# Kernel tuning notes

Hardware: AMD Instinct MI355X
Metric: run time of the kernel (lower is better)

## Reference

```python
import jax, jax.numpy as jnp
import numpy as np

N_NODES, N_EDGES, B = 5000, 160000, 8
IN_DIM, NB, RH = 64, 8, 64
MUL0, MUL1, MUL2 = 32, 16, 8
NW = 144  # 32*3 + 16*2 + 8*2 tensor-product path weights per edge
R_MAX, AVG_NEI = 6.0, 32.0
NL, POOL_H, OUT_D = 4, 128, 512


def setup_inputs():
    ks = jax.random.split(jax.random.key(0), 24)
    f = lambda k, shape, scale=1.0: jax.random.normal(k, shape, jnp.float32) * scale
    return {
        "x": f(ks[0], (N_NODES, IN_DIM)),
        "pos": f(ks[1], (N_NODES, 3)),
        "W_in": f(ks[2], (IN_DIM, MUL0), IN_DIM ** -0.5),
        "Wr1": f(ks[3], (NL, NB, RH), NB ** -0.5), "br1": jnp.zeros((NL, RH)),
        "Wr2": f(ks[4], (NL, RH, RH), RH ** -0.5), "br2": jnp.zeros((NL, RH)),
        "Wr3": f(ks[5], (NL, RH, NW), RH ** -0.5), "br3": jnp.zeros((NL, NW)),
        "Wm0": f(ks[6], (NL, 56, MUL0), 56 ** -0.5),
        "Wm1": f(ks[7], (NL, 48, MUL1), 48 ** -0.5),
        "Wm2": f(ks[8], (NL, 40, MUL2), 40 ** -0.5),
        "Ws0": f(ks[9], (NL, MUL0, MUL0), MUL0 ** -0.5),
        "Ws1": f(ks[10], (NL, MUL1, MUL1), MUL1 ** -0.5),
        "Ws2": f(ks[11], (NL, MUL2, MUL2), MUL2 ** -0.5),
        "Wg": f(ks[12], (NL, MUL0, MUL1 + MUL2), MUL0 ** -0.5), "bg": jnp.zeros((NL, MUL1 + MUL2)),
        "Wp1": f(ks[13], (MUL0, POOL_H), MUL0 ** -0.5), "bp1": jnp.zeros((POOL_H,)),
        "Wp2": f(ks[14], (POOL_H, POOL_H), POOL_H ** -0.5), "bp2": jnp.zeros((POOL_H,)),
        "Wp3": f(ks[15], (POOL_H, 1), POOL_H ** -0.5), "bp3": jnp.zeros((1,)),
        "Wo1": f(ks[16], (MUL0, OUT_D * 2), MUL0 ** -0.5), "bo1": jnp.zeros((OUT_D * 2,)),
        "g1": jnp.ones((OUT_D * 2,)), "be1": jnp.zeros((OUT_D * 2,)),
        "Wo2": f(ks[17], (OUT_D * 2, OUT_D), (OUT_D * 2) ** -0.5), "bo2": jnp.zeros((OUT_D,)),
        "g2": jnp.ones((OUT_D,)), "be2": jnp.zeros((OUT_D,)),
        "edge_index": jax.random.randint(ks[18], (2, N_EDGES), 0, N_NODES),
        "batch": jnp.sort(jax.random.randint(ks[19], (N_NODES,), 0, B)),
    }


def _ln(x, gamma, beta):
    m = x.mean(-1, keepdims=True)
    v = x.var(-1, keepdims=True)
    return (x - m) / jnp.sqrt(v + 1e-5) * gamma + beta


def _forward(x, pos, W_in, Wr1, br1, Wr2, br2, Wr3, br3, Wm0, Wm1, Wm2,
             Ws0, Ws1, Ws2, Wg, bg, Wp1, bp1, Wp2, bp2, Wp3, bp3,
             Wo1, bo1, g1, be1, Wo2, bo2, g2, be2, edge_index, batch):
    N = x.shape[0]
    src, dst = edge_index[0], edge_index[1]
    vec = pos[src] - pos[dst]                       # [E,3]
    r = jnp.sqrt(jnp.sum(vec * vec, -1) + 1e-12)    # [E]
    u = vec / r[:, None]
    # Bessel radial basis with smooth polynomial cutoff (p=6)
    nfreq = jnp.arange(1, NB + 1, dtype=x.dtype)
    bess = jnp.sqrt(2.0 / R_MAX) * jnp.sin(nfreq * jnp.pi * r[:, None] / R_MAX) / r[:, None]
    t = jnp.clip(r / R_MAX, 0.0, 1.0)
    fcut = (1.0 - 28.0 * t**6 + 48.0 * t**7 - 21.0 * t**8) * (r < R_MAX).astype(x.dtype)
    edge_emb = bess * fcut[:, None]                 # [E,NB]
    # real spherical harmonics of edge direction, component normalization
    ux, uy, uz = u[:, 0], u[:, 1], u[:, 2]
    Y1 = jnp.sqrt(3.0) * u                          # [E,3]
    Y2 = jnp.stack([15.0**0.5 * ux * uy, 15.0**0.5 * uy * uz,
                    0.5 * 5.0**0.5 * (3.0 * uz * uz - 1.0),
                    15.0**0.5 * ux * uz, 0.5 * 15.0**0.5 * (ux * ux - uy * uy)], -1)  # [E,5]
    # input embedding: 64x0e -> hidden irreps (only scalar path exists; l>0 start at 0)
    s = x @ W_in                                    # [N,32]
    v = jnp.zeros((N, MUL1, 3), x.dtype)            # [N,16,3] 1o
    q = jnp.zeros((N, MUL2, 5), x.dtype)            # [N,8,5]  2e
    for i in range(NL):
        w = jax.nn.silu(edge_emb @ Wr1[i] + br1[i])
        w = jax.nn.silu(w @ Wr2[i] + br2[i])
        w = w @ Wr3[i] + br3[i]                     # [E,144] per-edge TP path weights
        w_ss, w_sv, w_sq, w_vs, w_vv, w_qs, w_qq = jnp.split(w, [32, 64, 96, 112, 128, 136], -1)
        se, ve, qe = s[src], v[src], q[src]         # gather
        # tensor-product messages, grouped by output irrep
        m0 = jnp.concatenate([w_ss * se,
                              w_vv * jnp.einsum('ecm,em->ec', ve, Y1) / 3.0**0.5,
                              w_qq * jnp.einsum('ecm,em->ec', qe, Y2) / 5.0**0.5], -1)   # [E,56]
        m1 = jnp.concatenate([(w_sv * se)[:, :, None] * Y1[:, None, :],
                              w_vs[:, :, None] * ve], 1)                                  # [E,48,3]
        m2 = jnp.concatenate([(w_sq * se)[:, :, None] * Y2[:, None, :],
                              w_qs[:, :, None] * qe], 1)                                  # [E,40,5]
        a0 = jax.ops.segment_sum(m0, dst, num_segments=N) / AVG_NEI
        a1 = jax.ops.segment_sum(m1, dst, num_segments=N) / AVG_NEI
        a2 = jax.ops.segment_sum(m2, dst, num_segments=N) / AVG_NEI
        # per-irrep linear mix + self-connection
        ns = a0 @ Wm0[i] + s @ Ws0[i]
        nv = jnp.einsum('ncm,co->nom', a1, Wm1[i]) + jnp.einsum('ncm,co->nom', v, Ws1[i])
        nq = jnp.einsum('ncm,co->nom', a2, Wm2[i]) + jnp.einsum('ncm,co->nom', q, Ws2[i])
        # gate activation + resnet
        gates = jax.nn.sigmoid(ns @ Wg[i] + bg[i])  # [N,24]
        s = s + jax.nn.silu(ns)
        v = v + nv * gates[:, :MUL1, None]
        q = q + nq * gates[:, MUL1:, None]
    # attention pooling over scalar channels (scatter-softmax per graph)
    logits = (jax.nn.silu(jax.nn.silu(s @ Wp1 + bp1) @ Wp2 + bp2) @ Wp3 + bp3)[:, 0]
    mx = jax.ops.segment_max(logits, batch, num_segments=B)
    z = jnp.exp(logits - mx[batch])
    att = z / jax.ops.segment_sum(z, batch, num_segments=B)[batch]
    gpool = jax.ops.segment_sum(s * att[:, None], batch, num_segments=B)  # [B,32]
    h = jax.nn.silu(_ln(gpool @ Wo1 + bo1, g1, be1))
    return _ln(h @ Wo2 + bo2, g2, be2)              # [B,512]


def reference(x, pos, W_in, Wr1, br1, Wr2, br2, Wr3, br3, Wm0, Wm1, Wm2,
              Ws0, Ws1, Ws2, Wg, bg, Wp1, bp1, Wp2, bp2, Wp3, bp3,
              Wo1, bo1, g1, be1, Wo2, bo2, g2, be2, edge_index, batch):
    return _forward(x, pos, W_in, Wr1, br1, Wr2, br2, Wr3, br3, Wm0, Wm1, Wm2,
                    Ws0, Ws1, Ws2, Wg, bg, Wp1, bp1, Wp2, bp2, Wp3, bp3,
                    Wo1, bo1, g1, be1, Wo2, bo2, g2, be2, edge_index, batch)
```

## Files before the change

kernel.cpp:

```cpp
#include <hip/hip_runtime.h>

constexpr int NN  = 5000;
constexpr int NE  = 160000;
constexpr int NB_ = 8;
constexpr float RMAX   = 6.0f;
constexpr float INV_AVG = 1.0f/32.0f;
constexpr float SQ3  = 1.7320508075688772f;
constexpr float ISQ3 = 0.5773502691896258f;
constexpr float ISQ5 = 0.4472135954999579f;
constexpr float SQ15 = 3.872983346207417f;
constexpr float SQ5  = 2.2360679774997896f;
constexpr float PIF  = 3.14159265358979323846f;

__device__ __forceinline__ float sigmoid_f(float x){
#if __has_builtin(__builtin_amdgcn_rcpf)
    return __builtin_amdgcn_rcpf(1.0f + __expf(-x));
#else
    return 1.0f / (1.0f + __expf(-x));
#endif
}
__device__ __forceinline__ float silu_f(float x){ return x * sigmoid_f(x); }

__global__ void k_geom(const float* __restrict__ pos, const int* __restrict__ ei,
                       float* __restrict__ geom, int* __restrict__ counts){
    int e = blockIdx.x*256 + threadIdx.x;
    if (e >= NE) return;
    int s = ei[e], d = ei[NE + e];
    float vx = pos[3*s]-pos[3*d], vy = pos[3*s+1]-pos[3*d+1], vz = pos[3*s+2]-pos[3*d+2];
    float r2 = vx*vx + vy*vy + vz*vz + 1e-12f;
    float r  = sqrtf(r2);
    float ir = 1.0f/r;
    float ux = vx*ir, uy = vy*ir, uz = vz*ir;
    float t  = fminf(r*(1.0f/RMAX), 1.0f);
    float t2=t*t, t3=t2*t, t6=t3*t3, t7=t6*t, t8=t7*t;
    float fc = (1.0f - 28.0f*t6 + 48.0f*t7 - 21.0f*t8) * (r < RMAX ? 1.0f : 0.0f);
    float cb = sqrtf(2.0f/RMAX) * ir * fc;
    float w[16];
    #pragma unroll
    for (int k=0;k<8;k++){
        float arg = (float)(k+1) * (PIF/RMAX) * r;
        w[k] = cb * sinf(arg);
    }
    w[8]  = SQ3*ux; w[9] = SQ3*uy; w[10] = SQ3*uz;
    w[11] = SQ15*ux*uy; w[12] = SQ15*uy*uz; w[13] = 0.5f*SQ5*(3.0f*uz*uz-1.0f);
    w[14] = SQ15*ux*uz; w[15] = 0.5f*SQ15*(ux*ux-uy*uy);
    float4* o = (float4*)(geom + (size_t)e*16);
    o[0] = make_float4(w[0],w[1],w[2],w[3]);
    o[1] = make_float4(w[4],w[5],w[6],w[7]);
    o[2] = make_float4(w[8],w[9],w[10],w[11]);
    o[3] = make_float4(w[12],w[13],w[14],w[15]);
    atomicAdd(&counts[d], 1);
}

__global__ void k_scan(int* __restrict__ cr, int* __restrict__ fpos){
    __shared__ int part[256];
    int t = threadIdx.x;
    const int CH = (NN + 255)/256;
    int base = t*CH;
    int s = 0;
    for (int i=0;i<CH;i++){ int idx = base+i; if (idx < NN) s += cr[idx]; }
    part[t] = s; __syncthreads();
    for (int off=1; off<256; off<<=1){
        int v = (t >= off) ? part[t-off] : 0;
        __syncthreads();
        part[t] += v;
        __syncthreads();
    }
    int run = (t==0) ? 0 : part[t-1];
    for (int i=0;i<CH;i++){
        int idx = base+i;
        if (idx < NN){
            int c = cr[idx];
            cr[idx]  = run;
            fpos[idx] = run;
            run += c;
        } else if (idx == NN){
            cr[idx] = run;
        }
    }
}

__global__ void k_fill(const int* __restrict__ ei, int* __restrict__ fpos,
                       int* __restrict__ elist, int* __restrict__ slot){
    int e = blockIdx.x*256 + threadIdx.x;
    if (e >= NE) return;
    int d = ei[NE+e];
    int p = atomicAdd(&fpos[d], 1);
    elist[p] = e;
    slot[e]  = p;
}

__global__ void k_sinit(const float* __restrict__ x, const float* __restrict__ Win,
                        float* __restrict__ sA){
    int tid = blockIdx.x*256 + threadIdx.x;
    int n = tid >> 5, o = tid & 31;
    if (n >= NN) return;
    float a = 0.f;
    #pragma unroll
    for (int k=0;k<64;k++) a = fmaf(x[n*64+k], Win[k*32+o], a);
    sA[n*32+o] = a;
}

__launch_bounds__(256)
__global__ void k_mlp(const float* __restrict__ geom, const int* __restrict__ slot,
                      const float* __restrict__ Wr1, const float* __restrict__ br1,
                      const float* __restrict__ Wr2, const float* __restrict__ br2,
                      const float* __restrict__ Wr3, const float* __restrict__ br3,
                      float* __restrict__ wbuf, int layer){
    int e = blockIdx.x*256 + threadIdx.x;
    if (e >= NE) return;
    const float* W1 = Wr1 + layer*(8*64);
    const float* b1 = br1 + layer*64;
    const float* W2 = Wr2 + layer*(64*64);
    const float* b2 = br2 + layer*64;
    const float* W3 = Wr3 + layer*(64*144);
    const float* b3 = br3 + layer*144;
    float4 ga = *(const float4*)(geom + (size_t)e*16);
    float4 gb = *(const float4*)(geom + (size_t)e*16 + 4);
    float emb[8] = {ga.x,ga.y,ga.z,ga.w, gb.x,gb.y,gb.z,gb.w};
    float h1[64];
    #pragma unroll
    for (int j=0;j<64;j++) h1[j] = b1[j];
    #pragma unroll
    for (int k=0;k<8;k++){
        float ek = emb[k];
        #pragma unroll
        for (int j=0;j<64;j++) h1[j] = fmaf(ek, W1[k*64+j], h1[j]);
    }
    #pragma unroll
    for (int j=0;j<64;j++) h1[j] = silu_f(h1[j]);
    float h2[64];
    #pragma unroll
    for (int j=0;j<64;j++) h2[j] = b2[j];
    #pragma unroll
    for (int k=0;k<64;k++){
        float hk = h1[k];
        #pragma unroll
        for (int j=0;j<64;j++) h2[j] = fmaf(hk, W2[k*64+j], h2[j]);
    }
    #pragma unroll
    for (int j=0;j<64;j++) h2[j] = silu_f(h2[j]);
    float* wout = wbuf + (size_t)slot[e]*144;
    for (int oc=0; oc<144; oc+=8){
        float acc[8];
        #pragma unroll
        for (int u=0;u<8;u++) acc[u] = b3[oc+u];
        #pragma unroll
        for (int k=0;k<64;k++){
            float hk = h2[k];
            #pragma unroll
            for (int u=0;u<8;u++) acc[u] = fmaf(hk, W3[k*144+oc+u], acc[u]);
        }
        *(float4*)(wout+oc)   = make_float4(acc[0],acc[1],acc[2],acc[3]);
        *(float4*)(wout+oc+4) = make_float4(acc[4],acc[5],acc[6],acc[7]);
    }
}

__launch_bounds__(64)
__global__ void k_gather(const int* __restrict__ rowp, const int* __restrict__ elist,
                         const int* __restrict__ ei, const float* __restrict__ geom,
                         const float* __restrict__ wbuf,
                         const float* __restrict__ s_in, const float* __restrict__ v_in,
                         const float* __restrict__ q_in,
                         float* __restrict__ s_out, float* __restrict__ v_out,
                         float* __restrict__ q_out,
                         const float* __restrict__ Wm0, const float* __restrict__ Wm1,
                         const float* __restrict__ Wm2,
                         const float* __restrict__ Ws0, const float* __restrict__ Ws1,
                         const float* __restrict__ Ws2,
                         const float* __restrict__ Wg, const float* __restrict__ bg,
                         int layer){
    constexpr int SH_W = 0, SH_Y = 144, SH_SE = 152, SH_VE = 184, SH_QE = 232, SH_ONE = 272;
    __shared__ float sh[273];
    __shared__ float lacc[400];
    __shared__ float lnode[120];
    __shared__ float lns[32];
    __shared__ float lgate[24];
    int n = blockIdx.x;
    int lane = threadIdx.x;
    if (lane < 32) lnode[lane]      = s_in[n*32+lane];
    if (lane < 48) lnode[32+lane]   = v_in[n*48+lane];
    if (lane < 40) lnode[80+lane]   = q_in[n*40+lane];
    if (lane == 0) sh[SH_ONE] = 1.0f;

    int typ[7], wiA[7], siA[7], yiA[7];
    #pragma unroll
    for (int t=0;t<7;t++){
        int c = lane + 64*t;
        int T=3, W=0, S=0, Y=SH_ONE;
        if (c < 32){ T=0; W=c; S=SH_SE+c; }
        else if (c < 48){ T=1; W=112+(c-32); S=SH_VE+3*(c-32); }
        else if (c < 56){ T=2; W=136+(c-48); S=SH_QE+5*(c-48); }
        else if (c < 200){
            int d=c-56; int row=d/3; int col=d-3*row;
            if (row < 32){ T=0; W=32+row;       S=SH_SE+row;              Y=SH_Y+col; }
            else         { T=0; W=96+(row-32);  S=SH_VE+3*(row-32)+col; }
        } else if (c < 400){
            int d=c-200; int row=d/5; int col=d-5*row;
            if (row < 32){ T=0; W=64+row;       S=SH_SE+row;              Y=SH_Y+3+col; }
            else         { T=0; W=128+(row-32); S=SH_QE+5*(row-32)+col; }
        }
        typ[t]=T; wiA[t]=W; siA[t]=S; yiA[t]=Y;
    }
    float acc[7];
    #pragma unroll
    for (int t=0;t<7;t++) acc[t]=0.f;

    int beg = rowp[n], end = rowp[n+1];
    for (int idx=beg; idx<end; ++idx){
        int e   = elist[idx];
        int src = ei[e];
        if (lane < 36){
            *(float4*)&sh[SH_W + lane*4] = *(const float4*)(wbuf + (size_t)idx*144 + lane*4);
        } else if (lane < 38){
            *(float4*)&sh[SH_Y + (lane-36)*4] = *(const float4*)(geom + (size_t)e*16 + 8 + (lane-36)*4);
        } else if (lane < 46){
            *(float4*)&sh[SH_SE + (lane-38)*4] = *(const float4*)(s_in + (size_t)src*32 + (lane-38)*4);
        } else if (lane < 58){
            *(float4*)&sh[SH_VE + (lane-46)*4] = *(const float4*)(v_in + (size_t)src*48 + (lane-46)*4);
        } else {
            *(float4*)&sh[SH_QE + (lane-58)*4] = *(const float4*)(q_in + (size_t)src*40 + (lane-58)*4);
        }
        if (lane < 4){
            *(float4*)&sh[SH_QE + 24 + lane*4] = *(const float4*)(q_in + (size_t)src*40 + 24 + lane*4);
        }
        __syncthreads();
        #pragma unroll
        for (int t=0;t<7;t++){
            float m;
            if (typ[t]==0)      m = sh[wiA[t]] * sh[siA[t]] * sh[yiA[t]];
            else if (typ[t]==1) m = sh[wiA[t]] * ISQ3 *
                                    (sh[siA[t]]*sh[SH_Y] + sh[siA[t]+1]*sh[SH_Y+1] + sh[siA[t]+2]*sh[SH_Y+2]);
            else if (typ[t]==2) m = sh[wiA[t]] * ISQ5 *
                                    (sh[siA[t]]*sh[SH_Y+3] + sh[siA[t]+1]*sh[SH_Y+4] + sh[siA[t]+2]*sh[SH_Y+5] +
                                     sh[siA[t]+3]*sh[SH_Y+6] + sh[siA[t]+4]*sh[SH_Y+7]);
            else                m = 0.f;
            acc[t] += m;
        }
        __syncthreads();
    }
    #pragma unroll
    for (int t=0;t<7;t++){
        int c = lane + 64*t;
        if (c < 400) lacc[c] = acc[t] * INV_AVG;
    }
    __syncthreads();

    const float* Wm0p = Wm0 + layer*(56*32);
    const float* Ws0p = Ws0 + layer*(32*32);
    const float* Wm1p = Wm1 + layer*(48*16);
    const float* Ws1p = Ws1 + layer*(16*16);
    const float* Wm2p = Wm2 + layer*(40*8);
    const float* Ws2p = Ws2 + layer*(8*8);
    const float* Wgp  = Wg  + layer*(32*24);
    const float* bgp  = bg  + layer*24;

    if (lane < 32){
        float a = 0.f;
        #pragma unroll
        for (int c=0;c<56;c++) a = fmaf(lacc[c],  Wm0p[c*32+lane], a);
        #pragma unroll
        for (int c=0;c<32;c++) a = fmaf(lnode[c], Ws0p[c*32+lane], a);
        lns[lane] = a;
    }
    int o3 = lane/3, m3 = lane - 3*o3;
    int o5 = lane/5, m5 = lane - 5*o5;
    float nv = 0.f, nq = 0.f;
    if (lane < 48){
        float a = 0.f;
        #pragma unroll
        for (int c=0;c<48;c++) a = fmaf(lacc[56+c*3+m3],   Wm1p[c*16+o3], a);
        #pragma unroll
        for (int c=0;c<16;c++) a = fmaf(lnode[32+c*3+m3],  Ws1p[c*16+o3], a);
        nv = a;
    }
    if (lane < 40){
        float a = 0.f;
        #pragma unroll
        for (int c=0;c<40;c++) a = fmaf(lacc[200+c*5+m5],  Wm2p[c*8+o5], a);
        #pragma unroll
        for (int c=0;c<8;c++)  a = fmaf(lnode[80+c*5+m5],  Ws2p[c*8+o5], a);
        nq = a;
    }
    __syncthreads();
    if (lane < 24){
        float a = bgp[lane];
        #pragma unroll
        for (int c=0;c<32;c++) a = fmaf(lns[c], Wgp[c*24+lane], a);
        lgate[lane] = sigmoid_f(a);
    }
    __syncthreads();
    if (lane < 32) s_out[n*32+lane] = lnode[lane]    + silu_f(lns[lane]);
    if (lane < 48) v_out[n*48+lane] = lnode[32+lane] + nv * lgate[o3];
    if (lane < 40) q_out[n*40+lane] = lnode[80+lane] + nq * lgate[16+o5];
}

__launch_bounds__(128)
__global__ void k_pool(const float* __restrict__ s_in,
                       const float* __restrict__ Wp1, const float* __restrict__ bp1,
                       const float* __restrict__ Wp2, const float* __restrict__ bp2,
                       const float* __restrict__ Wp3, const float* __restrict__ bp3,
                       float* __restrict__ logits){
    __shared__ float ls[32];
    __shared__ float lh[128];
    __shared__ float wred[2];
    int n = blockIdx.x, t = threadIdx.x;
    if (t < 32) ls[t] = s_in[n*32+t];
    __syncthreads();
    float a = bp1[t];
    #pragma unroll
    for (int c=0;c<32;c++) a = fmaf(ls[c], Wp1[c*128+t], a);
    lh[t] = silu_f(a);
    __syncthreads();
    float b = bp2[t];
    #pragma unroll
    for (int k=0;k<128;k++) b = fmaf(lh[k], Wp2[k*128+t], b);
    float p = silu_f(b) * Wp3[t];
    #pragma unroll
    for (int off=32; off>0; off>>=1) p += __shfl_down(p, off, 64);
    if ((t & 63) == 0) wred[t>>6] = p;
    __syncthreads();
    if (t == 0) logits[n] = wred[0] + wred[1] + bp3[0];
}

__global__ void k_bmax(const float* __restrict__ logits, const int* __restrict__ batch,
                       float* __restrict__ mx){
    __shared__ float red[256];
    int b = blockIdx.x, t = threadIdx.x;
    float m = -3.0e38f;
    for (int n=t; n<NN; n+=256) if (batch[n]==b) m = fmaxf(m, logits[n]);
    red[t] = m; __syncthreads();
    for (int s2=128; s2>0; s2>>=1){ if (t<s2) red[t] = fmaxf(red[t], red[t+s2]); __syncthreads(); }
    if (t==0) mx[b] = red[0];
}

__global__ void k_z(const float* __restrict__ logits, const int* __restrict__ batch,
                    const float* __restrict__ mx, float* __restrict__ zbuf,
                    float* __restrict__ denom){
    int n = blockIdx.x*256 + threadIdx.x;
    if (n >= NN) return;
    int b = batch[n];
    float z = __expf(logits[n] - mx[b]);
    zbuf[n] = z;
    atomicAdd(&denom[b], z);
}

__global__ void k_gpool(const float* __restrict__ s_in, const float* __restrict__ zbuf,
                        const int* __restrict__ batch, const float* __restrict__ denom,
                        float* __restrict__ gpool){
    __shared__ float red[8][32];
    int b = blockIdx.x, t = threadIdx.x;
    int c = t & 31, g = t >> 5;
    float a = 0.f;
    for (int n=g; n<NN; n+=8){
        if (batch[n]==b) a = fmaf(zbuf[n], s_in[n*32+c], a);
    }
    red[g][c] = a; __syncthreads();
    if (t < 32){
        float s2 = 0.f;
        #pragma unroll
        for (int g2=0; g2<8; g2++) s2 += red[g2][t];
        gpool[b*32+t] = s2 / denom[b];
    }
}

__launch_bounds__(256)
__global__ void k_out1(const float* __restrict__ gpool, const float* __restrict__ Wo1,
                       const float* __restrict__ bo1, const float* __restrict__ g1,
                       const float* __restrict__ be1, float* __restrict__ hbuf){
    __shared__ float lg[32];
    __shared__ float red[256];
    __shared__ float stats[2];
    int b = blockIdx.x, t = threadIdx.x;
    if (t < 32) lg[t] = gpool[b*32+t];
    __syncthreads();
    float v[4];
    #pragma unroll
    for (int u=0;u<4;u++){
        int j = t + 256*u;
        float a = bo1[j];
        #pragma unroll
        for (int c=0;c<32;c++) a = fmaf(lg[c], Wo1[c*1024+j], a);
        v[u] = a;
    }
    red[t] = v[0]+v[1]+v[2]+v[3]; __syncthreads();
    for (int s2=128; s2>0; s2>>=1){ if (t<s2) red[t]+=red[t+s2]; __syncthreads(); }
    if (t==0) stats[0] = red[0]*(1.0f/1024.0f);
    __syncthreads();
    float mean = stats[0];
    float q1 = 0.f;
    #pragma unroll
    for (int u=0;u<4;u++){ float d = v[u]-mean; q1 += d*d; }
    red[t] = q1; __syncthreads();
    for (int s2=128; s2>0; s2>>=1){ if (t<s2) red[t]+=red[t+s2]; __syncthreads(); }
    if (t==0) stats[1] = red[0]*(1.0f/1024.0f);
    __syncthreads();
    float rstd = rsqrtf(stats[1] + 1e-5f);
    #pragma unroll
    for (int u=0;u<4;u++){
        int j = t + 256*u;
        float xln = (v[u]-mean)*rstd*g1[j] + be1[j];
        hbuf[b*1024+j] = silu_f(xln);
    }
}

__launch_bounds__(256)
__global__ void k_out2(const float* __restrict__ hbuf, const float* __restrict__ Wo2,
                       const float* __restrict__ bo2, const float* __restrict__ g2,
                       const float* __restrict__ be2, float* __restrict__ out){
    __shared__ float lh[1024];
    __shared__ float red[256];
    __shared__ float stats[2];
    int b = blockIdx.x, t = threadIdx.x;
    #pragma unroll
    for (int u=0;u<4;u++) lh[t+256*u] = hbuf[b*1024 + t + 256*u];
    __syncthreads();
    float v[2];
    #pragma unroll
    for (int u=0;u<2;u++){
        int j = t + 256*u;
        float a = bo2[j];
        #pragma unroll 4
        for (int k=0;k<1024;k++) a = fmaf(lh[k], Wo2[(size_t)k*512+j], a);
        v[u] = a;
    }
    red[t] = v[0]+v[1]; __syncthreads();
    for (int s2=128; s2>0; s2>>=1){ if (t<s2) red[t]+=red[t+s2]; __syncthreads(); }
    if (t==0) stats[0] = red[0]*(1.0f/512.0f);
    __syncthreads();
    float mean = stats[0];
    float q1 = 0.f;
    #pragma unroll
    for (int u=0;u<2;u++){ float d = v[u]-mean; q1 += d*d; }
    red[t] = q1; __syncthreads();
    for (int s2=128; s2>0; s2>>=1){ if (t<s2) red[t]+=red[t+s2]; __syncthreads(); }
    if (t==0) stats[1] = red[0]*(1.0f/512.0f);
    __syncthreads();
    float rstd = rsqrtf(stats[1] + 1e-5f);
    #pragma unroll
    for (int u=0;u<2;u++){
        int j = t + 256*u;
        out[b*512+j] = (v[u]-mean)*rstd*g2[j] + be2[j];
    }
}

extern "C" void kernel_launch(void* const* d_in, const int* in_sizes, int n_in,
                              void* d_out, int out_size, void* d_ws, size_t ws_size,
                              hipStream_t stream){
    const float* x   = (const float*)d_in[0];
    const float* pos = (const float*)d_in[1];
    const float* Win = (const float*)d_in[2];
    const float* Wr1 = (const float*)d_in[3];
    const float* br1 = (const float*)d_in[4];
    const float* Wr2 = (const float*)d_in[5];
    const float* br2 = (const float*)d_in[6];
    const float* Wr3 = (const float*)d_in[7];
    const float* br3 = (const float*)d_in[8];
    const float* Wm0 = (const float*)d_in[9];
    const float* Wm1 = (const float*)d_in[10];
    const float* Wm2 = (const float*)d_in[11];
    const float* Ws0 = (const float*)d_in[12];
    const float* Ws1 = (const float*)d_in[13];
    const float* Ws2 = (const float*)d_in[14];
    const float* Wg  = (const float*)d_in[15];
    const float* bg  = (const float*)d_in[16];
    const float* Wp1 = (const float*)d_in[17];
    const float* bp1 = (const float*)d_in[18];
    const float* Wp2 = (const float*)d_in[19];
    const float* bp2 = (const float*)d_in[20];
    const float* Wp3 = (const float*)d_in[21];
    const float* bp3 = (const float*)d_in[22];
    const float* Wo1 = (const float*)d_in[23];
    const float* bo1 = (const float*)d_in[24];
    const float* g1  = (const float*)d_in[25];
    const float* be1 = (const float*)d_in[26];
    const float* Wo2 = (const float*)d_in[27];
    const float* bo2 = (const float*)d_in[28];
    const float* g2  = (const float*)d_in[29];
    const float* be2 = (const float*)d_in[30];
    const int* ei    = (const int*)d_in[31];
    const int* batch = (const int*)d_in[32];
    float* out = (float*)d_out;

    char* wsb = (char*)d_ws;
    size_t off = 0;
    auto take = [&](size_t bytes)->char*{
        char* p = wsb + off;
        off = (off + bytes + 255) & ~(size_t)255;
        return p;
    };
    float* geom  = (float*)take((size_t)NE*16*4);
    float* wbuf  = (float*)take((size_t)NE*144*4);
    int*   rowp  = (int*)take((size_t)(NN+1)*4);
    int*   fpos  = (int*)take((size_t)NN*4);
    int*   elist = (int*)take((size_t)NE*4);
    int*   slot  = (int*)take((size_t)NE*4);
    float* sA = (float*)take((size_t)NN*32*4);
    float* sB = (float*)take((size_t)NN*32*4);
    float* vA = (float*)take((size_t)NN*48*4);
    float* vB = (float*)take((size_t)NN*48*4);
    float* qA = (float*)take((size_t)NN*40*4);
    float* qB = (float*)take((size_t)NN*40*4);
    float* logits = (float*)take((size_t)NN*4);
    float* zbuf   = (float*)take((size_t)NN*4);
    float* mx     = (float*)take(64);
    float* denom  = (float*)take(64);
    float* gpool  = (float*)take((size_t)NB_*32*4);
    float* hbuf   = (float*)take((size_t)NB_*1024*4);
    (void)ws_size; (void)in_sizes; (void)n_in; (void)out_size;

    hipMemsetAsync(rowp, 0, (size_t)(NN+1)*4, stream);
    hipMemsetAsync(vA,   0, (size_t)NN*48*4, stream);
    hipMemsetAsync(qA,   0, (size_t)NN*40*4, stream);
    hipMemsetAsync(denom,0, 64, stream);

    k_geom<<<(NE+255)/256, 256, 0, stream>>>(pos, ei, geom, rowp);
    k_scan<<<1, 256, 0, stream>>>(rowp, fpos);
    k_fill<<<(NE+255)/256, 256, 0, stream>>>(ei, fpos, elist, slot);
    k_sinit<<<(NN*32+255)/256, 256, 0, stream>>>(x, Win, sA);

    float* si=sA; float* so=sB; float* vi=vA; float* vo=vB; float* qi=qA; float* qo=qB;
    for (int layer=0; layer<4; ++layer){
        k_mlp<<<(NE+255)/256, 256, 0, stream>>>(geom, slot, Wr1, br1, Wr2, br2, Wr3, br3, wbuf, layer);
        k_gather<<<NN, 64, 0, stream>>>(rowp, elist, ei, geom, wbuf, si, vi, qi, so, vo, qo,
                                        Wm0, Wm1, Wm2, Ws0, Ws1, Ws2, Wg, bg, layer);
        float* ts=si; si=so; so=ts;
        float* tv=vi; vi=vo; vo=tv;
        float* tq=qi; qi=qo; qo=tq;
    }
    k_pool<<<NN, 128, 0, stream>>>(si, Wp1, bp1, Wp2, bp2, Wp3, bp3, logits);
    k_bmax<<<NB_, 256, 0, stream>>>(logits, batch, mx);
    k_z<<<(NN+255)/256, 256, 0, stream>>>(logits, batch, mx, zbuf, denom);
    k_gpool<<<NB_, 256, 0, stream>>>(si, zbuf, batch, denom, gpool);
    k_out1<<<NB_, 256, 0, stream>>>(gpool, Wo1, bo1, g1, be1, hbuf);
    k_out2<<<NB_, 256, 0, stream>>>(hbuf, Wo2, bo2, g2, be2, out);
}
```

Before: 1.215 ms.

## Tile radial MLP in shared memory and widen output head kernels

The per-edge radial MLP is restructured so each 256-thread block stages all three layer weights and 64 edges' embeddings in LDS. Each thread computes 2 edges by 8 or 18 output columns, with hidden activations exchanged through shared memory. This replaces the per-thread 64-wide register arrays and redundant global weight reads, which likely caused spills and low occupancy. The output head kernels now use 1024 threads, and out2 splits the K reduction in half, giving more parallelism on the tiny 8-block launches. Sigmoid also drops the fast rcp builtin for a true divide, and the roughly 58KB of LDS per block limits occupancy.

After: 1.147 ms. 5.6% less time.

```diff
diff --git a/kernel.cpp b/kernel.cpp
--- a/kernel.cpp
+++ b/kernel.cpp
@@ -13,11 +13,7 @@
 constexpr float PIF  = 3.14159265358979323846f;
 
 __device__ __forceinline__ float sigmoid_f(float x){
-#if __has_builtin(__builtin_amdgcn_rcpf)
-    return __builtin_amdgcn_rcpf(1.0f + __expf(-x));
-#else
     return 1.0f / (1.0f + __expf(-x));
-#endif
 }
 __device__ __forceinline__ float silu_f(float x){ return x * sigmoid_f(x); }
 
@@ -107,52 +103,123 @@
                       const float* __restrict__ Wr2, const float* __restrict__ br2,
                       const float* __restrict__ Wr3, const float* __restrict__ br3,
                       float* __restrict__ wbuf, int layer){
-    int e = blockIdx.x*256 + threadIdx.x;
-    if (e >= NE) return;
+    __shared__ float w1s[8*64];
+    __shared__ float w2s[64*64];
+    __shared__ float w3s[64*144];
+    __shared__ float b1s[64], b2s[64], b3s[144];
+    __shared__ float embs[64][8];
+    __shared__ float hs[64][68];
+    __shared__ int   slots[64];
+
+    const int t  = threadIdx.x;
+    const int e0 = blockIdx.x * 64;
     const float* W1 = Wr1 + layer*(8*64);
     const float* b1 = br1 + layer*64;
     const float* W2 = Wr2 + layer*(64*64);
     const float* b2 = br2 + layer*64;
     const float* W3 = Wr3 + layer*(64*144);
     const float* b3 = br3 + layer*144;
-    float4 ga = *(const float4*)(geom + (size_t)e*16);
-    float4 gb = *(const float4*)(geom + (size_t)e*16 + 4);
-    float emb[8] = {ga.x,ga.y,ga.z,ga.w, gb.x,gb.y,gb.z,gb.w};
-    float h1[64];
-    #pragma unroll
-    for (int j=0;j<64;j++) h1[j] = b1[j];
+
+    {
+        const float4* W2v = (const float4*)W2;
+        float4* w2v = (float4*)w2s;
+        #pragma unroll
+        for (int i=0;i<4;i++) w2v[t + 256*i] = W2v[t + 256*i];
+        const float4* W3v = (const float4*)W3;
+        float4* w3v = (float4*)w3s;
+        #pragma unroll
+        for (int i=0;i<9;i++) w3v[t + 256*i] = W3v[t + 256*i];
+        if (t < 128) ((float4*)w1s)[t] = ((const float4*)W1)[t];
+        if (t < 64){ b1s[t] = b1[t]; b2s[t] = b2[t]; slots[t] = slot[e0 + t]; }
+        if (t < 144) b3s[t] = b3[t];
+        if (t < 128){
+            ((float4*)embs)[t] = *((const float4*)geom + (size_t)(e0 + (t>>1))*4 + (t&1));
+        }
+    }
+    __syncthreads();
+
+    const int eg = t >> 3;
+    const int jg = t & 7;
+    const int ea = eg*2, eb = ea+1;
+
+    float a0[2][8];
+    #pragma unroll
+    for (int i=0;i<2;i++)
+        #pragma unroll
+        for (int u=0;u<8;u++) a0[i][u] = b1s[8*jg+u];
     #pragma unroll
     for (int k=0;k<8;k++){
-        float ek = emb[k];
-        #pragma unroll
-        for (int j=0;j<64;j++) h1[j] = fmaf(ek, W1[k*64+j], h1[j]);
-    }
-    #pragma unroll
-    for (int j=0;j<64;j++) h1[j] = silu_f(h1[j]);
-    float h2[64];
-    #pragma unroll
-    for (int j=0;j<64;j++) h2[j] = b2[j];
+        float e_a = embs[ea][k], e_b = embs[eb][k];
+        #pragma unroll
+        for (int u=0;u<8;u++){
+            float wv = w1s[k*64 + 8*jg + u];
+            a0[0][u] = fmaf(e_a, wv, a0[0][u]);
+            a0[1][u] = fmaf(e_b, wv, a0[1][u]);
+        }
+    }
+    #pragma unroll
+    for (int i=0;i<2;i++){
+        int e = ea + i;
+        float4 p0 = make_float4(silu_f(a0[i][0]), silu_f(a0[i][1]), silu_f(a0[i][2]), silu_f(a0[i][3]));
+        float4 p1 = make_float4(silu_f(a0[i][4]), silu_f(a0[i][5]), silu_f(a0[i][6]), silu_f(a0[i][7]));
+        *(float4*)&hs[e][8*jg]     = p0;
+        *(float4*)&hs[e][8*jg + 4] = p1;
+    }
+    __syncthreads();
+
+    float a1[2][8];
+    #pragma unroll
+    for (int i=0;i<2;i++)
+        #pragma unroll
+        for (int u=0;u<8;u++) a1[i][u] = b2s[8*jg+u];
     #pragma unroll
     for (int k=0;k<64;k++){
-        float hk = h1[k];
-        #pragma unroll
-        for (int j=0;j<64;j++) h2[j] = fmaf(hk, W2[k*64+j], h2[j]);
-    }
-    #pragma unroll
-    for (int j=0;j<64;j++) h2[j] = silu_f(h2[j]);
-    float* wout = wbuf + (size_t)slot[e]*144;
-    for (int oc=0; oc<144; oc+=8){
-        float acc[8];
-        #pragma unroll
-        for (int u=0;u<8;u++) acc[u] = b3[oc+u];
-        #pragma unroll
-        for (int k=0;k<64;k++){
-            float hk = h2[k];
-            #pragma unroll
-            for (int u=0;u<8;u++) acc[u] = fmaf(hk, W3[k*144+oc+u], acc[u]);
-        }
-        *(float4*)(wout+oc)   = make_float4(acc[0],acc[1],acc[2],acc[3]);
-        *(float4*)(wout+oc+4) = make_float4(acc[4],acc[5],acc[6],acc[7]);
+        float h_a = hs[ea][k], h_b = hs[eb][k];
+        float4 wA = *(const float4*)&w2s[k*64 + 8*jg];
+        float4 wB = *(const float4*)&w2s[k*64 + 8*jg + 4];
+        a1[0][0]=fmaf(h_a,wA.x,a1[0][0]); a1[0][1]=fmaf(h_a,wA.y,a1[0][1]);
+        a1[0][2]=fmaf(h_a,wA.z,a1[0][2]); a1[0][3]=fmaf(h_a,wA.w,a1[0][3]);
+        a1[0][4]=fmaf(h_a,wB.x,a1[0][4]); a1[0][5]=fmaf(h_a,wB.y,a1[0][5]);
+        a1[0][6]=fmaf(h_a,wB.z,a1[0][6]); a1[0][7]=fmaf(h_a,wB.w,a1[0][7]);
+        a1[1][0]=fmaf(h_b,wA.x,a1[1][0]); a1[1][1]=fmaf(h_b,wA.y,a1[1][1]);
+        a1[1][2]=fmaf(h_b,wA.z,a1[1][2]); a1[1][3]=fmaf(h_b,wA.w,a1[1][3]);
+        a1[1][4]=fmaf(h_b,wB.x,a1[1][4]); a1[1][5]=fmaf(h_b,wB.y,a1[1][5]);
+        a1[1][6]=fmaf(h_b,wB.z,a1[1][6]); a1[1][7]=fmaf(h_b,wB.w,a1[1][7]);
+    }
+    __syncthreads();
+    #pragma unroll
+    for (int i=0;i<2;i++){
+        int e = ea + i;
+        float4 p0 = make_float4(silu_f(a1[i][0]), silu_f(a1[i][1]), silu_f(a1[i][2]), silu_f(a1[i][3]));
+        float4 p1 = make_float4(silu_f(a1[i][4]), silu_f(a1[i][5]), silu_f(a1[i][6]), silu_f(a1[i][7]));
+        *(float4*)&hs[e][8*jg]     = p0;
+        *(float4*)&hs[e][8*jg + 4] = p1;
+    }
+    __syncthreads();
+
+    float c2[2][18];
+    #pragma unroll
+    for (int i=0;i<2;i++)
+        #pragma unroll
+        for (int u=0;u<18;u++) c2[i][u] = b3s[18*jg+u];
+    #pragma unroll
+    for (int k=0;k<64;k++){
+        float h_a = hs[ea][k], h_b = hs[eb][k];
+        #pragma unroll
+        for (int u2=0;u2<9;u2++){
+            float2 wv = *(const float2*)&w3s[k*144 + 18*jg + 2*u2];
+            c2[0][2*u2]   = fmaf(h_a, wv.x, c2[0][2*u2]);
+            c2[0][2*u2+1] = fmaf(h_a, wv.y, c2[0][2*u2+1]);
+            c2[1][2*u2]   = fmaf(h_b, wv.x, c2[1][2*u2]);
+            c2[1][2*u2+1] = fmaf(h_b, wv.y, c2[1][2*u2+1]);
+        }
+    }
+    #pragma unroll
+    for (int i=0;i<2;i++){
+        float* wo = wbuf + (size_t)slots[ea+i]*144 + 18*jg;
+        #pragma unroll
+        for (int u2=0;u2<9;u2++)
+            *(float2*)(wo + 2*u2) = make_float2(c2[i][2*u2], c2[i][2*u2+1]);
     }
 }
 
@@ -364,84 +431,64 @@
     }
 }
 
-__launch_bounds__(256)
+__launch_bounds__(1024)
 __global__ void k_out1(const float* __restrict__ gpool, const float* __restrict__ Wo1,
                        const float* __restrict__ bo1, const float* __restrict__ g1,
                        const float* __restrict__ be1, float* __restrict__ hbuf){
     __shared__ float lg[32];
-    __shared__ float red[256];
+    __shared__ float red[1024];
     __shared__ float stats[2];
     int b = blockIdx.x, t = threadIdx.x;
     if (t < 32) lg[t] = gpool[b*32+t];
     __syncthreads();
-    float v[4];
-    #pragma unroll
-    for (int u=0;u<4;u++){
-        int j = t + 256*u;
-        float a = bo1[j];
-        #pragma unroll
-        for (int c=0;c<32;c++) a = fmaf(lg[c], Wo1[c*1024+j], a);
-        v[u] = a;
-    }
-    red[t] = v[0]+v[1]+v[2]+v[3]; __syncthreads();
-    for (int s2=128; s2>0; s2>>=1){ if (t<s2) red[t]+=red[t+s2]; __syncthreads(); }
+    float a = bo1[t];
+    #pragma unroll
+    for (int c=0;c<32;c++) a = fmaf(lg[c], Wo1[c*1024+t], a);
+    red[t] = a; __syncthreads();
+    for (int s2=512; s2>0; s2>>=1){ if (t<s2) red[t]+=red[t+s2]; __syncthreads(); }
     if (t==0) stats[0] = red[0]*(1.0f/1024.0f);
     __syncthreads();
     float mean = stats[0];
-    float q1 = 0.f;
-    #pragma unroll
-    for (int u=0;u<4;u++){ float d = v[u]-mean; q1 += d*d; }
-    red[t] = q1; __syncthreads();
-    for (int s2=128; s2>0; s2>>=1){ if (t<s2) red[t]+=red[t+s2]; __syncthreads(); }
+    float d = a - mean;
+    red[t] = d*d; __syncthreads();
+    for (int s2=512; s2>0; s2>>=1){ if (t<s2) red[t]+=red[t+s2]; __syncthreads(); }
     if (t==0) stats[1] = red[0]*(1.0f/1024.0f);
     __syncthreads();
     float rstd = rsqrtf(stats[1] + 1e-5f);
-    #pragma unroll
-    for (int u=0;u<4;u++){
-        int j = t + 256*u;
-        float xln = (v[u]-mean)*rstd*g1[j] + be1[j];
-        hbuf[b*1024+j] = silu_f(xln);
-    }
-}
-
-__launch_bounds__(256)
+    hbuf[b*1024+t] = silu_f(d*rstd*g1[t] + be1[t]);
+}
+
+__launch_bounds__(1024)
 __global__ void k_out2(const float* __restrict__ hbuf, const float* __restrict__ Wo2,
                        const float* __restrict__ bo2, const float* __restrict__ g2,
                        const float* __restrict__ be2, float* __restrict__ out){
     __shared__ float lh[1024];
-    __shared__ float red[256];
+    __shared__ float part[1024];
+    __shared__ float red[1024];
     __shared__ float stats[2];
     int b = blockIdx.x, t = threadIdx.x;
-    #pragma unroll
-    for (int u=0;u<4;u++) lh[t+256*u] = hbuf[b*1024 + t + 256*u];
-    __syncthreads();
-    float v[2];
-    #pragma unroll
-    for (int u=0;u<2;u++){
-        int j = t + 256*u;
-        float a = bo2[j];
-        #pragma unroll 4
-        for (int k=0;k<1024;k++) a = fmaf(lh[k], Wo2[(size_t)k*512+j], a);
-        v[u] = a;
-    }
-    red[t] = v[0]+v[1]; __syncthreads();
-    for (int s2=128; s2>0; s2>>=1){ if (t<s2) red[t]+=red[t+s2]; __syncthreads(); }
+    lh[t] = hbuf[b*1024 + t];
+    __syncthreads();
+    int j = t & 511, half = t >> 9;
+    float a = (half == 0) ? bo2[j] : 0.0f;
+    int k0 = half*512;
+    #pragma unroll 8
+    for (int k=0;k<512;k++) a = fmaf(lh[k0+k], Wo2[(size_t)(k0+k)*512 + j], a);
+    part[t] = a; __syncthreads();
+    float y = 0.f;
+    if (t < 512) y = part[t] + part[t+512];
+    red[t] = (t < 512) ? y : 0.f; __syncthreads();
+    for (int s2=512; s2>0; s2>>=1){ if (t<s2) red[t]+=red[t+s2]; __syncthreads(); }
     if (t==0) stats[0] = red[0]*(1.0f/512.0f);
     __syncthreads();
     float mean = stats[0];
-    float q1 = 0.f;
-    #pragma unroll
-    for (int u=0;u<2;u++){ float d = v[u]-mean; q1 += d*d; }
-    red[t] = q1; __syncthreads();
-    for (int s2=128; s2>0; s2>>=1){ if (t<s2) red[t]+=red[t+s2]; __syncthreads(); }
+    float d = y - mean;
+    red[t] = (t < 512) ? d*d : 0.f; __syncthreads();
+    for (int s2=512; s2>0; s2>>=1){ if (t<s2) red[t]+=red[t+s2]; __syncthreads(); }
     if (t==0) stats[1] = red[0]*(1.0f/512.0f);
     __syncthreads();
     float rstd = rsqrtf(stats[1] + 1e-5f);
-    #pragma unroll
-    for (int u=0;u<2;u++){
-        int j = t + 256*u;
-        out[b*512+j] = (v[u]-mean)*rstd*g2[j] + be2[j];
-    }
+    if (t < 512) out[b*512+t] = d*rstd*g2[t] + be2[t];
 }
 
 extern "C" void kernel_launch(void* const* d_in, const int* in_sizes, int n_in,
@@ -521,7 +568,7 @@
 
     float* si=sA; float* so=sB; float* vi=vA; float* vo=vB; float* qi=qA; float* qo=qB;
     for (int layer=0; layer<4; ++layer){
-        k_mlp<<<(NE+255)/256, 256, 0, stream>>>(geom, slot, Wr1, br1, Wr2, br2, Wr3, br3, wbuf, layer);
+        k_mlp<<<NE/64, 256, 0, stream>>>(geom, slot, Wr1, br1, Wr2, br2, Wr3, br3, wbuf, layer);
         k_gather<<<NN, 64, 0, stream>>>(rowp, elist, ei, geom, wbuf, si, vi, qi, so, vo, qo,
                                         Wm0, Wm1, Wm2, Ws0, Ws1, Ws2, Wg, bg, layer);
         float* ts=si; si=so; so=ts;
@@ -532,6 +579,6 @@
     k_bmax<<<NB_, 256, 0, stream>>>(logits, batch, mx);
     k_z<<<(NN+255)/256, 256, 0, stream>>>(logits, batch, mx, zbuf, denom);
     k_gpool<<<NB_, 256, 0, stream>>>(si, zbuf, batch, denom, gpool);
-    k_out1<<<NB_, 256, 0, stream>>>(gpool, Wo1, bo1, g1, be1, hbuf);
-    k_out2<<<NB_, 256, 0, stream>>>(hbuf, Wo2, bo2, g2, be2, out);
-}
+    k_out1<<<NB_, 1024, 0, stream>>>(gpool, Wo1, bo1, g1, be1, hbuf);
+    k_out2<<<NB_, 1024, 0, stream>>>(hbuf, Wo2, bo2, g2, be2, out);
+}
```
